# Performance work log

Measured on AMD Instinct MI355X. Metric: run time of the kernel, lower is better.

Reference implementation:

```python
import jax, jax.numpy as jnp
import numpy as np

N_NODES = 50000
N_EDGES = 600000
N_GRAPHS = 100
IN_DIM, HID, OUT = 128, 128, 64
K = 2  # DGL TAGConv default hop count


def setup_inputs() -> dict:
    key = jax.random.key(0)
    ks = jax.random.split(key, 8)
    x = jax.random.normal(ks[0], (N_NODES, IN_DIM), dtype=jnp.float32)
    src = jax.random.randint(ks[1], (N_EDGES,), 0, N_NODES)
    dst = jax.random.randint(ks[2], (N_EDGES,), 0, N_NODES)
    graph_id = jnp.sort(jax.random.randint(ks[3], (N_NODES,), 0, N_GRAPHS))
    # TAGConv lin: Linear(in_feats*(K+1), out_feats), stored as (in*(K+1), out)
    W1 = jax.random.normal(ks[4], (IN_DIM * (K + 1), HID), dtype=jnp.float32) / np.sqrt(IN_DIM * (K + 1))
    b1 = jnp.zeros((HID,), dtype=jnp.float32)
    W2 = jax.random.normal(ks[5], (HID * (K + 1), OUT), dtype=jnp.float32) / np.sqrt(HID * (K + 1))
    b2 = jnp.zeros((OUT,), dtype=jnp.float32)
    return {"x": x, "W1": W1, "b1": b1, "W2": W2, "b2": b2,
            "src": src, "dst": dst, "graph_id": graph_id}


def _tagconv(h, src, dst, norm, W, b):
    """DGL TAGConv: relu(concat_k (D^-1/2 A D^-1/2)^k h @ W + b), k=0..K."""
    feats = [h]
    cur = h
    for _ in range(K):
        cur = cur * norm[:, None]
        cur = jax.ops.segment_sum(cur[src], dst, num_segments=N_NODES)
        cur = cur * norm[:, None]
        feats.append(cur)
    out = jnp.concatenate(feats, axis=-1) @ W + b
    return jax.nn.relu(out)


def reference(x, W1, b1, W2, b2, src, dst, graph_id):
    # symmetric norm from in-degrees (clamped to 1), as in DGL TAGConv
    deg = jax.ops.segment_sum(jnp.ones_like(dst, dtype=x.dtype), dst, num_segments=N_NODES)
    norm = jnp.clip(deg, 1.0, None) ** -0.5
    h = _tagconv(x, src, dst, norm, W1, b1)
    h = _tagconv(h, src, dst, norm, W2, b2)
    # MaxPooling readout: per-graph max over nodes
    return jax.ops.segment_max(h, graph_id, num_segments=N_GRAPHS)
```

## Files before the change

### kernel.cpp

```cpp
#include <hip/hip_runtime.h>
#include <hip/hip_bf16.h>

#define N_NODES 50000
#define N_EDGES 600000
#define N_GRAPHS 100
#define M_PAD 50176
#define TSLICE ((size_t)M_PAD * 32)

typedef __bf16 bf16_t;
typedef __attribute__((ext_vector_type(8))) __bf16 bf16x8;
typedef __attribute__((ext_vector_type(4))) __bf16 bf16x4;
typedef __attribute__((ext_vector_type(4))) float f32x4;

__global__ void degk(const int* __restrict__ dst, int* __restrict__ deg,
                     int* __restrict__ rank, int n) {
    int i = blockIdx.x * 256 + threadIdx.x;
    if (i < n) rank[i] = atomicAdd(&deg[dst[i]], 1);
}

__global__ __launch_bounds__(1024) void scan1(const int* __restrict__ deg,
                                              int* __restrict__ row_off,
                                              int* __restrict__ partial,
                                              float* __restrict__ norm, int n) {
    __shared__ int buf[1024];
    int i = blockIdx.x * 1024 + threadIdx.x;
    int v = (i < n) ? deg[i] : 0;
    buf[threadIdx.x] = v;
    __syncthreads();
    for (int off = 1; off < 1024; off <<= 1) {
        int t = (threadIdx.x >= off) ? buf[threadIdx.x - off] : 0;
        __syncthreads();
        buf[threadIdx.x] += t;
        __syncthreads();
    }
    if (i < n) {
        row_off[i + 1] = buf[threadIdx.x];
        float d = fmaxf((float)v, 1.0f);
        norm[i] = 1.0f / sqrtf(d);
    }
    if (threadIdx.x == 1023) partial[blockIdx.x] = buf[1023];
}

__global__ __launch_bounds__(256) void scan3(int* __restrict__ row_off,
                                             const int* __restrict__ partial, int n) {
    int i = blockIdx.x * 256 + threadIdx.x;
    int c = (blockIdx.x * 256) >> 10;
    __shared__ int pre;
    if (threadIdx.x < 64) {
        int v = (threadIdx.x < c) ? partial[threadIdx.x] : 0;
        for (int off = 32; off; off >>= 1) v += __shfl_down(v, off, 64);
        if (threadIdx.x == 0) pre = v;
    }
    __syncthreads();
    if (i == 0) row_off[0] = 0;
    if (i < n) row_off[i + 1] += pre;
}

#define NPRE 6250
#define NSC  ((N_EDGES + 255) / 256)
#define NPW  ((384 * 192 + 255) / 256)
__global__ __launch_bounds__(256) void midk(const float* __restrict__ x,
                                            const float* __restrict__ norm,
                                            bf16_t* __restrict__ xb, bf16_t* __restrict__ xs,
                                            const int* __restrict__ src, const int* __restrict__ dst,
                                            const int* __restrict__ row_off,
                                            const int* __restrict__ rank,
                                            int* __restrict__ csr_src,
                                            const float* __restrict__ W1, bf16_t* __restrict__ Wp1,
                                            const float* __restrict__ W2, bf16_t* __restrict__ Wp2) {
    int b = blockIdx.x;
    if (b < NPRE) {
        int i = b * 256 + threadIdx.x;
        int node = i >> 5, c4 = i & 31;
        float4 v = *(const float4*)(x + (size_t)node * 128 + c4 * 4);
        float nd = norm[node];
        bf16x4 ob, os;
        ob[0] = (bf16_t)v.x; ob[1] = (bf16_t)v.y; ob[2] = (bf16_t)v.z; ob[3] = (bf16_t)v.w;
        os[0] = (bf16_t)(v.x * nd); os[1] = (bf16_t)(v.y * nd);
        os[2] = (bf16_t)(v.z * nd); os[3] = (bf16_t)(v.w * nd);
        size_t t = (size_t)(c4 >> 3) * TSLICE + (size_t)node * 32 + (c4 & 7) * 4;
        *(bf16x4*)(xb + t) = ob;
        *(bf16x4*)(xs + t) = os;
    } else if (b < NPRE + NSC) {
        int e = (b - NPRE) * 256 + threadIdx.x;
        if (e >= N_EDGES) return;
        int d = dst[e];
        csr_src[row_off[d] + rank[e]] = src[e];
    } else {
        int i = (b - NPRE - NSC) * 256 + threadIdx.x;
        if (i < 384 * 128) {
            int k = i >> 7, n = i & 127;
            int kt = k >> 5, q = (k >> 3) & 3, j = k & 7;
            int nt = n >> 4, ln = n & 15;
            Wp1[(((size_t)kt * 8 + nt) * 64 + q * 16 + ln) * 8 + j] = (bf16_t)W1[i];
        } else if (i < 384 * 128 + 384 * 64) {
            int idx = i - 384 * 128;
            int k384 = idx >> 6, n = idx & 63;
            int blk = k384 >> 7, kk = k384 & 127;
            int col = blk * 64 + n;
            int kt = kk >> 5, q = (kk >> 3) & 3, j = kk & 7;
            int nt = col >> 4, ln = col & 15;
            Wp2[(((size_t)kt * 12 + nt) * 64 + q * 16 + ln) * 8 + j] = (bf16_t)W2[idx];
        }
    }
}

template <int TILES, bool SCALED>
__global__ __launch_bounds__(256) void spmm8(const bf16_t* __restrict__ in,
                                             bf16_t* __restrict__ out_c,
                                             bf16_t* __restrict__ out_s,
                                             const float* __restrict__ norm,
                                             const int* __restrict__ row_off,
                                             const int* __restrict__ csr, int n) {
    constexpr int PARTS = 8 / TILES;
    int bid  = blockIdx.x;
    int xcd  = bid & 7;
    int tile = xcd / PARTS;
    int part = xcd % PARTS;
    int sub  = bid >> 3;
    int grp  = threadIdx.x >> 3;
    int half = (threadIdx.x >> 2) & 1;
    int l    = threadIdx.x & 3;
    int node = (sub * PARTS + part) * 32 + grp;
    if (node >= n) return;
    int e0 = row_off[node], e1 = row_off[node + 1];
    const bf16_t* base = in + (size_t)tile * TSLICE + l * 8;
    float acc[8] = {};
    if (e0 < e1) {
        int be   = e0 + half;
        int cnt  = (e1 - be + 1) >> 1;
        int emax = e1 - 1;
        int s[8];
#pragma unroll
        for (int k = 0; k < 8; k++) s[k] = csr[min(be + 2 * k, emax)];
        bf16x8 v[8];
#pragma unroll
        for (int k = 0; k < 8; k++) v[k] = *(const bf16x8*)(base + (size_t)s[k] * 32);
#pragma unroll
        for (int k = 0; k < 8; k++) {
            float wk = (k < cnt) ? 1.0f : 0.0f;
#pragma unroll
            for (int j = 0; j < 8; j++) acc[j] += wk * (float)v[k][j];
        }
        for (int e = be + 16; e < e1; e += 2) {
            int ss = csr[e];
            bf16x8 vv = *(const bf16x8*)(base + (size_t)ss * 32);
#pragma unroll
            for (int j = 0; j < 8; j++) acc[j] += (float)vv[j];
        }
    }
#pragma unroll
    for (int j = 0; j < 8; j++) acc[j] += __shfl_xor(acc[j], 4, 64);
    float nd = norm[node];
    size_t t = (size_t)tile * TSLICE + (size_t)node * 32 + l * 8;
    if (half == 0) {
        bf16x8 oc;
#pragma unroll
        for (int j = 0; j < 8; j++) oc[j] = (bf16_t)(acc[j] * nd);
        __builtin_nontemporal_store(oc, (bf16x8*)(out_c + t));
    } else if (SCALED) {
        float n2 = nd * nd;
        bf16x8 os;
#pragma unroll
        for (int j = 0; j < 8; j++) os[j] = (bf16_t)(acc[j] * n2);
        __builtin_nontemporal_store(os, (bf16x8*)(out_s + t));
    }
}

__global__ __launch_bounds__(256) void gemm1k(const bf16_t* __restrict__ f0,
                                              const bf16_t* __restrict__ f1,
                                              const bf16_t* __restrict__ f2,
                                              const bf16_t* __restrict__ Wp,
                                              const float* __restrict__ bias,
                                              bf16_t* __restrict__ outb, int M) {
    int wave = threadIdx.x >> 6;
    int lane = threadIdx.x & 63;
    int q = lane >> 4, ln = lane & 15;
    int row0 = blockIdx.x * 128 + wave * 32;

    f32x4 acc[2][8] = {};
    const bf16_t* feats[3] = {f0, f1, f2};
    const bf16x8* Wf = (const bf16x8*)Wp;

#pragma unroll
    for (int kc = 0; kc < 12; kc++) {
        const bf16_t* A = feats[kc >> 2] + (size_t)(kc & 3) * TSLICE + q * 8;
        bf16x8 a0 = *(const bf16x8*)(A + (size_t)(row0 + ln) * 32);
        bf16x8 a1 = *(const bf16x8*)(A + (size_t)(row0 + 16 + ln) * 32);
        const bf16x8* Bp = Wf + (size_t)kc * 8 * 64 + lane;
#pragma unroll
        for (int nt = 0; nt < 8; nt++) {
            bf16x8 b = Bp[nt * 64];
            acc[0][nt] = __builtin_amdgcn_mfma_f32_16x16x32_bf16(a0, b, acc[0][nt], 0, 0, 0);
            acc[1][nt] = __builtin_amdgcn_mfma_f32_16x16x32_bf16(a1, b, acc[1][nt], 0, 0, 0);
        }
    }

    float bv[8];
#pragma unroll
    for (int nt = 0; nt < 8; nt++) bv[nt] = bias[nt * 16 + ln];

#pragma unroll
    for (int mt = 0; mt < 2; mt++) {
#pragma unroll
        for (int r = 0; r < 4; r++) {
            int row = row0 + mt * 16 + q * 4 + r;
            if (row >= M) continue;
#pragma unroll
            for (int nt = 0; nt < 8; nt++) {
                float val = fmaxf(acc[mt][nt][r] + bv[nt], 0.f);
                outb[(size_t)(nt >> 1) * TSLICE + (size_t)row * 32 + (nt & 1) * 16 + ln] = (bf16_t)val;
            }
        }
    }
}

__global__ __launch_bounds__(256) void gemm2k(const bf16_t* __restrict__ h,
                                              const bf16_t* __restrict__ Wp,
                                              const float* __restrict__ bias,
                                              const float* __restrict__ norm,
                                              float* __restrict__ t0,
                                              bf16_t* __restrict__ uvs, int M) {
    int wave = threadIdx.x >> 6;
    int lane = threadIdx.x & 63;
    int q = lane >> 4, ln = lane & 15;
    int row0 = blockIdx.x * 128 + wave * 32;

    f32x4 acc[2][12] = {};
    const bf16x8* Wf = (const bf16x8*)Wp;

#pragma unroll
    for (int kc = 0; kc < 4; kc++) {
        const bf16_t* A = h + (size_t)kc * TSLICE + q * 8;
        bf16x8 a0 = *(const bf16x8*)(A + (size_t)(row0 + ln) * 32);
        bf16x8 a1 = *(const bf16x8*)(A + (size_t)(row0 + 16 + ln) * 32);
        const bf16x8* Bp = Wf + (size_t)kc * 12 * 64 + lane;
#pragma unroll
        for (int nt = 0; nt < 12; nt++) {
            bf16x8 b = Bp[nt * 64];
            acc[0][nt] = __builtin_amdgcn_mfma_f32_16x16x32_bf16(a0, b, acc[0][nt], 0, 0, 0);
            acc[1][nt] = __builtin_amdgcn_mfma_f32_16x16x32_bf16(a1, b, acc[1][nt], 0, 0, 0);
        }
    }

    float bv[4];
#pragma unroll
    for (int nt = 0; nt < 4; nt++) bv[nt] = bias[nt * 16 + ln];

#pragma unroll
    for (int mt = 0; mt < 2; mt++) {
#pragma unroll
        for (int r = 0; r < 4; r++) {
            int row = row0 + mt * 16 + q * 4 + r;
            if (row >= M) continue;
            float nd = norm[row];
#pragma unroll
            for (int nt = 0; nt < 4; nt++)
                __builtin_nontemporal_store(acc[mt][nt][r] + bv[nt],
                                            t0 + (size_t)row * 64 + nt * 16 + ln);
#pragma unroll
            for (int nt = 4; nt < 12; nt++) {
                int col = (nt - 4) * 16 + ln;
                uvs[(size_t)(col >> 5) * TSLICE + (size_t)row * 32 + (col & 31)] =
                    (bf16_t)(acc[mt][nt][r] * nd);
            }
        }
    }
}

__global__ __launch_bounds__(256) void finpool(const float* __restrict__ t0,
                                               const bf16_t* __restrict__ Au,
                                               const bf16_t* __restrict__ A2v,
                                               const int* __restrict__ gid,
                                               unsigned int* __restrict__ out, int n) {
    int wave = threadIdx.x >> 6;
    int lane = threadIdx.x & 63;
    int n0 = blockIdx.x * 256 + wave * 64;
    if (n0 >= n) return;
    int n1 = min(n0 + 64, n);
    size_t cb = (size_t)(lane >> 5) * TSLICE + (lane & 31);
    int cur = gid[n0];
    float m = 0.f;
    for (int i = n0; i < n1; i++) {
        int g = gid[i];
        float v = fmaxf(t0[(size_t)i * 64 + lane]
                        + (float)Au[cb + (size_t)i * 32]
                        + (float)A2v[cb + (size_t)i * 32], 0.f);
        if (g != cur) { atomicMax(&out[cur * 64 + lane], __float_as_uint(m)); cur = g; m = v; }
        else m = fmaxf(m, v);
    }
    atomicMax(&out[cur * 64 + lane], __float_as_uint(m));
}

extern "C" void kernel_launch(void* const* d_in, const int* in_sizes, int n_in,
                              void* d_out, int out_size, void* d_ws, size_t ws_size,
                              hipStream_t stream) {
    const float* x  = (const float*)d_in[0];
    const float* W1 = (const float*)d_in[1];
    const float* b1 = (const float*)d_in[2];
    const float* W2 = (const float*)d_in[3];
    const float* b2 = (const float*)d_in[4];
    const int* src  = (const int*)d_in[5];
    const int* dst  = (const int*)d_in[6];
    const int* gid  = (const int*)d_in[7];
    float* out = (float*)d_out;

    char* ws = (char*)d_ws;
    size_t off = 0;
    auto take = [&](size_t bytes) {
        void* p = ws + off;
        off = (off + bytes + 255) & ~(size_t)255;
        return p;
    };
    int* deg     = (int*)take((size_t)N_NODES * 4);
    size_t zero_bytes = off;
    float* norm  = (float*)take((size_t)N_NODES * 4);
    int* row_off = (int*)take((size_t)(N_NODES + 1) * 4);
    int* partial = (int*)take(64 * 4);
    int* rank    = (int*)take((size_t)N_EDGES * 4);
    int* csr_src = (int*)take((size_t)N_EDGES * 4);
    bf16_t* Wp1  = (bf16_t*)take((size_t)384 * 128 * 2);
    bf16_t* Wp2  = (bf16_t*)take((size_t)384 * 64 * 2);
    bf16_t* B0 = (bf16_t*)take((size_t)M_PAD * 128 * 2);
    bf16_t* B1 = (bf16_t*)take((size_t)M_PAD * 128 * 2);
    bf16_t* B2 = (bf16_t*)take((size_t)M_PAD * 128 * 2);
    bf16_t* B3 = (bf16_t*)take((size_t)M_PAD * 128 * 2);
    bf16_t* B4 = (bf16_t*)take((size_t)M_PAD * 128 * 2);
    bf16_t* B5 = (bf16_t*)take((size_t)M_PAD * 128 * 2);
    float*  B6 = (float*)take((size_t)M_PAD * 64 * 4);
    bf16_t* B7 = (bf16_t*)take((size_t)M_PAD * 128 * 2);
    bf16_t* B8 = (bf16_t*)take((size_t)M_PAD * 128 * 2);
    bf16_t* B9 = (bf16_t*)take((size_t)M_PAD * 128 * 2);
    bf16_t* B10= (bf16_t*)take((size_t)M_PAD * 128 * 2);
    (void)ws_size; (void)in_sizes; (void)n_in; (void)out_size;

    hipMemsetAsync(d_ws, 0, zero_bytes, stream);
    hipMemsetAsync(d_out, 0, (size_t)N_GRAPHS * 64 * 4, stream);

    degk<<<(N_EDGES + 255) / 256, 256, 0, stream>>>(dst, deg, rank, N_EDGES);
    int nchunks = (N_NODES + 1023) / 1024;
    scan1<<<nchunks, 1024, 0, stream>>>(deg, row_off, partial, norm, N_NODES);
    scan3<<<(N_NODES + 255) / 256, 256, 0, stream>>>(row_off, partial, N_NODES);
    midk<<<NPRE + NSC + NPW, 256, 0, stream>>>(x, norm, B0, B1, src, dst, row_off, rank,
                                               csr_src, W1, Wp1, W2, Wp2);

    int grid4 = 8 * ((N_NODES + 63) / 64);
    int grid2 = 8 * ((N_NODES + 127) / 128);
    int gemm_grid = M_PAD / 128;

    spmm8<4, true ><<<grid4, 256, 0, stream>>>(B1, B2, B3, norm, row_off, csr_src, N_NODES);
    spmm8<4, false><<<grid4, 256, 0, stream>>>(B3, B4, nullptr, norm, row_off, csr_src, N_NODES);
    gemm1k<<<gemm_grid, 256, 0, stream>>>(B0, B2, B4, Wp1, b1, B5, N_NODES);
    gemm2k<<<gemm_grid, 256, 0, stream>>>(B5, Wp2, b2, norm, B6, B7, N_NODES);
    spmm8<4, true ><<<grid4, 256, 0, stream>>>(B7, B8, B9, norm, row_off, csr_src, N_NODES);
    spmm8<2, false><<<grid2, 256, 0, stream>>>(B9 + 2 * TSLICE, B10, nullptr, norm, row_off, csr_src, N_NODES);
    finpool<<<(N_NODES + 255) / 256, 256, 0, stream>>>(B6, B8, B10, gid, (unsigned int*)out, N_NODES);
}
```

Before: 284.2 us.

## Widen feature tiles from 32 to 64 columns across SpMM, GEMMs and pooling

```diff
diff --git a/kernel.cpp b/kernel.cpp
--- a/kernel.cpp
+++ b/kernel.cpp
@@ -5,7 +5,7 @@
 #define N_EDGES 600000
 #define N_GRAPHS 100
 #define M_PAD 50176
-#define TSLICE ((size_t)M_PAD * 32)
+#define TS64 ((size_t)M_PAD * 64)
 
 typedef __bf16 bf16_t;
 typedef __attribute__((ext_vector_type(8))) __bf16 bf16x8;
@@ -78,7 +78,7 @@
         ob[0] = (bf16_t)v.x; ob[1] = (bf16_t)v.y; ob[2] = (bf16_t)v.z; ob[3] = (bf16_t)v.w;
         os[0] = (bf16_t)(v.x * nd); os[1] = (bf16_t)(v.y * nd);
         os[2] = (bf16_t)(v.z * nd); os[3] = (bf16_t)(v.w * nd);
-        size_t t = (size_t)(c4 >> 3) * TSLICE + (size_t)node * 32 + (c4 & 7) * 4;
+        size_t t = (size_t)(c4 >> 4) * TS64 + (size_t)node * 64 + (c4 & 15) * 4;
         *(bf16x4*)(xb + t) = ob;
         *(bf16x4*)(xs + t) = os;
     } else if (b < NPRE + NSC) {
@@ -106,25 +106,25 @@
 }
 
 template <int TILES, bool SCALED>
-__global__ __launch_bounds__(256) void spmm8(const bf16_t* __restrict__ in,
-                                             bf16_t* __restrict__ out_c,
-                                             bf16_t* __restrict__ out_s,
-                                             const float* __restrict__ norm,
-                                             const int* __restrict__ row_off,
-                                             const int* __restrict__ csr, int n) {
-    constexpr int PARTS = 8 / TILES;
+__global__ __launch_bounds__(256) void spmm16(const bf16_t* __restrict__ in,
+                                              bf16_t* __restrict__ out_c,
+                                              bf16_t* __restrict__ out_s,
+                                              const float* __restrict__ norm,
+                                              const int* __restrict__ row_off,
+                                              const int* __restrict__ csr, int n) {
+    constexpr int PARTS = 8 / (TILES * 2) * 2;
     int bid  = blockIdx.x;
     int xcd  = bid & 7;
     int tile = xcd / PARTS;
     int part = xcd % PARTS;
     int sub  = bid >> 3;
-    int grp  = threadIdx.x >> 3;
-    int half = (threadIdx.x >> 2) & 1;
-    int l    = threadIdx.x & 3;
-    int node = (sub * PARTS + part) * 32 + grp;
+    int grp  = threadIdx.x >> 4;
+    int half = (threadIdx.x >> 3) & 1;
+    int l    = threadIdx.x & 7;
+    int node = (sub * PARTS + part) * 16 + grp;
     if (node >= n) return;
     int e0 = row_off[node], e1 = row_off[node + 1];
-    const bf16_t* base = in + (size_t)tile * TSLICE + l * 8;
+    const bf16_t* base = in + (size_t)tile * TS64 + l * 8;
     float acc[8] = {};
     if (e0 < e1) {
         int be   = e0 + half;
@@ -135,7 +135,7 @@
         for (int k = 0; k < 8; k++) s[k] = csr[min(be + 2 * k, emax)];
         bf16x8 v[8];
 #pragma unroll
-        for (int k = 0; k < 8; k++) v[k] = *(const bf16x8*)(base + (size_t)s[k] * 32);
+        for (int k = 0; k < 8; k++) v[k] = *(const bf16x8*)(base + (size_t)s[k] * 64);
 #pragma unroll
         for (int k = 0; k < 8; k++) {
             float wk = (k < cnt) ? 1.0f : 0.0f;
@@ -144,15 +144,15 @@
         }
         for (int e = be + 16; e < e1; e += 2) {
             int ss = csr[e];
-            bf16x8 vv = *(const bf16x8*)(base + (size_t)ss * 32);
+            bf16x8 vv = *(const bf16x8*)(base + (size_t)ss * 64);
 #pragma unroll
             for (int j = 0; j < 8; j++) acc[j] += (float)vv[j];
         }
     }
 #pragma unroll
-    for (int j = 0; j < 8; j++) acc[j] += __shfl_xor(acc[j], 4, 64);
+    for (int j = 0; j < 8; j++) acc[j] += __shfl_xor(acc[j], 8, 64);
     float nd = norm[node];
-    size_t t = (size_t)tile * TSLICE + (size_t)node * 32 + l * 8;
+    size_t t = (size_t)tile * TS64 + (size_t)node * 64 + l * 8;
     if (half == 0) {
         bf16x8 oc;
 #pragma unroll
@@ -184,9 +184,10 @@
 
 #pragma unroll
     for (int kc = 0; kc < 12; kc++) {
-        const bf16_t* A = feats[kc >> 2] + (size_t)(kc & 3) * TSLICE + q * 8;
-        bf16x8 a0 = *(const bf16x8*)(A + (size_t)(row0 + ln) * 32);
-        bf16x8 a1 = *(const bf16x8*)(A + (size_t)(row0 + 16 + ln) * 32);
+        int c = kc & 3;
+        const bf16_t* A = feats[kc >> 2] + (size_t)(c >> 1) * TS64 + (c & 1) * 32 + q * 8;
+        bf16x8 a0 = *(const bf16x8*)(A + (size_t)(row0 + ln) * 64);
+        bf16x8 a1 = *(const bf16x8*)(A + (size_t)(row0 + 16 + ln) * 64);
         const bf16x8* Bp = Wf + (size_t)kc * 8 * 64 + lane;
 #pragma unroll
         for (int nt = 0; nt < 8; nt++) {
@@ -209,7 +210,7 @@
 #pragma unroll
             for (int nt = 0; nt < 8; nt++) {
                 float val = fmaxf(acc[mt][nt][r] + bv[nt], 0.f);
-                outb[(size_t)(nt >> 1) * TSLICE + (size_t)row * 32 + (nt & 1) * 16 + ln] = (bf16_t)val;
+                outb[(size_t)(nt >> 2) * TS64 + (size_t)row * 64 + (nt & 3) * 16 + ln] = (bf16_t)val;
             }
         }
     }
@@ -231,9 +232,9 @@
 
 #pragma unroll
     for (int kc = 0; kc < 4; kc++) {
-        const bf16_t* A = h + (size_t)kc * TSLICE + q * 8;
-        bf16x8 a0 = *(const bf16x8*)(A + (size_t)(row0 + ln) * 32);
-        bf16x8 a1 = *(const bf16x8*)(A + (size_t)(row0 + 16 + ln) * 32);
+        const bf16_t* A = h + (size_t)(kc >> 1) * TS64 + (kc & 1) * 32 + q * 8;
+        bf16x8 a0 = *(const bf16x8*)(A + (size_t)(row0 + ln) * 64);
+        bf16x8 a1 = *(const bf16x8*)(A + (size_t)(row0 + 16 + ln) * 64);
         const bf16x8* Bp = Wf + (size_t)kc * 12 * 64 + lane;
 #pragma unroll
         for (int nt = 0; nt < 12; nt++) {
@@ -260,8 +261,8 @@
                                             t0 + (size_t)row * 64 + nt * 16 + ln);
 #pragma unroll
             for (int nt = 4; nt < 12; nt++) {
-                int col = (nt - 4) * 16 + ln;
-                uvs[(size_t)(col >> 5) * TSLICE + (size_t)row * 32 + (col & 31)] =
+                int m = nt - 4;
+                uvs[(size_t)(m >> 2) * TS64 + (size_t)row * 64 + (m & 3) * 16 + ln] =
                     (bf16_t)(acc[mt][nt][r] * nd);
             }
         }
@@ -278,14 +279,13 @@
     int n0 = blockIdx.x * 256 + wave * 64;
     if (n0 >= n) return;
     int n1 = min(n0 + 64, n);
-    size_t cb = (size_t)(lane >> 5) * TSLICE + (lane & 31);
     int cur = gid[n0];
     float m = 0.f;
     for (int i = n0; i < n1; i++) {
         int g = gid[i];
         float v = fmaxf(t0[(size_t)i * 64 + lane]
-                        + (float)Au[cb + (size_t)i * 32]
-                        + (float)A2v[cb + (size_t)i * 32], 0.f);
+                        + (float)Au[(size_t)i * 64 + lane]
+                        + (float)A2v[(size_t)i * 64 + lane], 0.f);
         if (g != cur) { atomicMax(&out[cur * 64 + lane], __float_as_uint(m)); cur = g; m = v; }
         else m = fmaxf(m, v);
     }
@@ -331,7 +331,7 @@
     bf16_t* B7 = (bf16_t*)take((size_t)M_PAD * 128 * 2);
     bf16_t* B8 = (bf16_t*)take((size_t)M_PAD * 128 * 2);
     bf16_t* B9 = (bf16_t*)take((size_t)M_PAD * 128 * 2);
-    bf16_t* B10= (bf16_t*)take((size_t)M_PAD * 128 * 2);
+    bf16_t* B10= (bf16_t*)take((size_t)M_PAD * 64 * 2);
     (void)ws_size; (void)in_sizes; (void)n_in; (void)out_size;
 
     hipMemsetAsync(d_ws, 0, zero_bytes, stream);
@@ -344,15 +344,15 @@
     midk<<<NPRE + NSC + NPW, 256, 0, stream>>>(x, norm, B0, B1, src, dst, row_off, rank,
                                                csr_src, W1, Wp1, W2, Wp2);
 
-    int grid4 = 8 * ((N_NODES + 63) / 64);
-    int grid2 = 8 * ((N_NODES + 127) / 128);
+    int grid2t = 8 * ((N_NODES + 63) / 64);
+    int grid1t = 8 * ((N_NODES + 127) / 128);
     int gemm_grid = M_PAD / 128;
 
-    spmm8<4, true ><<<grid4, 256, 0, stream>>>(B1, B2, B3, norm, row_off, csr_src, N_NODES);
-    spmm8<4, false><<<grid4, 256, 0, stream>>>(B3, B4, nullptr, norm, row_off, csr_src, N_NODES);
+    spmm16<2, true ><<<grid2t, 256, 0, stream>>>(B1, B2, B3, norm, row_off, csr_src, N_NODES);
+    spmm16<2, false><<<grid2t, 256, 0, stream>>>(B3, B4, nullptr, norm, row_off, csr_src, N_NODES);
     gemm1k<<<gemm_grid, 256, 0, stream>>>(B0, B2, B4, Wp1, b1, B5, N_NODES);
     gemm2k<<<gemm_grid, 256, 0, stream>>>(B5, Wp2, b2, norm, B6, B7, N_NODES);
-    spmm8<4, true ><<<grid4, 256, 0, stream>>>(B7, B8, B9, norm, row_off, csr_src, N_NODES);
-    spmm8<2, false><<<grid2, 256, 0, stream>>>(B9 + 2 * TSLICE, B10, nullptr, norm, row_off, csr_src, N_NODES);
+    spmm16<2, true ><<<grid2t, 256, 0, stream>>>(B7, B8, B9, norm, row_off, csr_src, N_NODES);
+    spmm16<1, false><<<grid1t, 256, 0, stream>>>(B9 + TS64, B10, nullptr, norm, row_off, csr_src, N_NODES);
     finpool<<<(N_NODES + 255) / 256, 256, 0, stream>>>(B6, B8, B10, gid, (unsigned int*)out, N_NODES);
 }
```

Measured after the change: 286.3 us. No clear change (+0.7%).
